# Kernel optimization log

Hardware: AMD Instinct MI355X
Metric: run time of the kernel (lower is better)

Reference implementation:

```python
import jax, jax.numpy as jnp
import numpy as np

B, T, C = 8, 2048, 1024  # micro_bsz, seq_len, n_embd (== complexsize)


def setup_inputs() -> dict:
    key = jax.random.key(0)
    ks = jax.random.split(key, 6)
    w = lambda k, shape: (jax.random.normal(k, shape, dtype=jnp.float32) * 0.02)
    return {
        "x": jax.random.normal(ks[0], (B, T, C), dtype=jnp.float32),
        "Wk": w(ks[1], (2 * C, C)),      # key: n_embd -> 2*n_embd (no bias)
        "Wa": w(ks[2], (C, 2 * C)),      # activation: 2*n_embd -> n_embd (no bias)
        "Wf": w(ks[3], (2, C, C)),       # WaveNet filter conv, kernel=2, WIO layout
        "Wg": w(ks[4], (2, C, C)),       # WaveNet gate conv, kernel=2, WIO layout
        "Wo": w(ks[5], (C, C)),          # WaveNet 1x1 output projection
    }


def _causal_conv(x, W):
    # x: [B,T,Cin], W: [K,Cin,Cout]; left-pad K-1 for causality
    return jax.lax.conv_general_dilated(
        x, W, window_strides=(1,), padding=[(W.shape[0] - 1, 0)],
        dimension_numbers=("NWC", "WIO", "NWC"))


def _wavenet_short(x, Wf, Wg, Wo):
    # undialated gated WaveNet unit: tanh(conv_f(x)) * sigmoid(conv_g(x)) -> 1x1 proj
    h = jnp.tanh(_causal_conv(x, Wf)) * jax.nn.sigmoid(_causal_conv(x, Wg))
    return h @ Wo.T


def reference(x, Wk, Wa, Wf, Wg, Wo):
    Bx, Tx, Cx = x.shape
    k = (x @ Wk.T).reshape(Bx, Tx, Cx, 2)                 # [B,T,C,2]
    cv = jax.lax.complex(k[..., 0], k[..., 1])            # view_as_complex -> [B,T,C]
    scale = jax.lax.cummax(jnp.abs(cv), axis=1)           # running max of magnitude
    cv2 = cv / scale.astype(cv.dtype)                      # normalize magnitude <= 1
    kv = jnp.cumprod(cv2, axis=1)                          # complex cumulative product
    re = jnp.stack([kv.real, kv.imag], axis=-1).reshape(Bx, Tx, 2 * Cx)  # view_as_real
    return (re @ Wa.T) * _wavenet_short(x * scale, Wf, Wg, Wo)
```

## Files before the change

### kernel.cpp

```cpp
#include <hip/hip_runtime.h>
#include <cmath>

#define T_SEQ 2048
#define C_DIM 1024
#define BM 128
#define BN 128
#define BK 32

typedef unsigned short u16;
typedef unsigned int u32;
typedef short bf16x8 __attribute__((ext_vector_type(8)));
typedef _Float16 f16x8 __attribute__((ext_vector_type(8)));
typedef float f32x4 __attribute__((ext_vector_type(4)));
typedef unsigned short u16x8 __attribute__((ext_vector_type(8)));

#define AS1 __attribute__((address_space(1)))
#define AS3 __attribute__((address_space(3)))

__device__ __forceinline__ u16 f2bf(float f) {
    u32 u = __builtin_bit_cast(u32, f);
    u32 r = u + 0x7fffu + ((u >> 16) & 1u);
    return (u16)(r >> 16);
}
__device__ __forceinline__ u16 f2h(float f) {
    return __builtin_bit_cast(u16, (_Float16)f);
}
__device__ __forceinline__ float h2f(u16 h) {
    return (float)__builtin_bit_cast(_Float16, h);
}
__device__ __forceinline__ void gl_lds16(const void* g, void* l) {
    __builtin_amdgcn_global_load_lds((const AS1 u32*)g, (AS3 u32*)l, 16, 0, 0);
}

__device__ __forceinline__ int xcd_swz(int lin, int nwg) {
    return (lin & 7) * (nwg >> 3) + (lin >> 3);
}

#define SBAR() do { __builtin_amdgcn_sched_barrier(0); \
                    __builtin_amdgcn_s_barrier(); \
                    __builtin_amdgcn_sched_barrier(0); } while (0)
#define VMC(n) do { asm volatile("s_waitcnt vmcnt(" #n ")" ::: "memory"); \
                    __builtin_amdgcn_sched_barrier(0); } while (0)
#define LGKM0() do { asm volatile("s_waitcnt lgkmcnt(0)" ::: "memory"); \
                     __builtin_amdgcn_sched_barrier(0); } while (0)

__global__ __launch_bounds__(512, 2)
void gemm8(const u16* __restrict__ Ap, const u16* __restrict__ Bp,
           u16* __restrict__ Cout, int M, int N, int K)
{
    __shared__ u16 lds[2 * 32768];
    const int tid  = threadIdx.x;
    const int lane = tid & 63;
    const int wid  = tid >> 6;
    const int wrow = wid >> 2;
    const int wcol = wid & 3;
    const int gx = gridDim.x;
    const int lin = xcd_swz(blockIdx.x + gx * blockIdx.y, gx * gridDim.y);
    const int m0 = (lin / gx) * 256;
    const int n0 = (lin % gx) * 256;
    const int NT = K / 64;

    f32x4 acc[8][4] = {};

    auto stageu = [&](int t, int u) {
        const int isB = u & 1, kh = u >> 1;
        u16* ubase = &lds[(t & 1) * 32768 + isB * 16384 + kh * 8192];
        const u16* src = isB ? Bp + (size_t)n0 * K : Ap + (size_t)m0 * K;
        const int k0 = t * 64 + kh * 32;
        #pragma unroll
        for (int j = 0; j < 2; ++j) {
            const int c = wid + 8 * j;
            const int p = c * 64 + lane;
            const int row = p >> 2;
            const int sp  = (p & 3) ^ ((row >> 1) & 3);
            gl_lds16(src + (size_t)row * K + k0 + sp * 8, ubase + c * 512);
        }
    };

    auto lda = [&](int buf, int kh, int mq, f16x8 (&a)[4]) {
        const u16* base = &lds[buf * 32768 + kh * 8192];
        #pragma unroll
        for (int f = 0; f < 4; ++f) {
            const int row = wrow * 128 + mq * 64 + f * 16 + (lane & 15);
            const int sp  = (lane >> 4) ^ ((row >> 1) & 3);
            a[f] = *(const f16x8*)&base[row * 32 + sp * 8];
        }
    };
    auto ldb = [&](int buf, int kh, f16x8 (&b)[4]) {
        const u16* base = &lds[buf * 32768 + 16384 + kh * 8192];
        #pragma unroll
        for (int f = 0; f < 4; ++f) {
            const int row = wcol * 64 + f * 16 + (lane & 15);
            const int sp  = (lane >> 4) ^ ((row >> 1) & 3);
            b[f] = *(const f16x8*)&base[row * 32 + sp * 8];
        }
    };
    auto mm = [&](const f16x8 (&a)[4], const f16x8 (&b)[4], int mq) {
        __builtin_amdgcn_s_setprio(1);
        #pragma unroll
        for (int fm = 0; fm < 4; ++fm)
            #pragma unroll
            for (int fn = 0; fn < 4; ++fn)
                acc[mq * 4 + fm][fn] = __builtin_amdgcn_mfma_f32_16x16x32_f16(
                    a[fm], b[fn], acc[mq * 4 + fm][fn], 0, 0, 0);
        __builtin_amdgcn_s_setprio(0);
    };

    stageu(0, 0); stageu(0, 1); stageu(0, 2); stageu(0, 3);
    VMC(0);
    SBAR();

    f16x8 a[4], b[4];
    for (int t = 0; t < NT; ++t) {
        const int buf = t & 1;
        const bool more = (t + 1 < NT);
        lda(buf, 0, 0, a); ldb(buf, 0, b);
        if (more) stageu(t + 1, 0);
        SBAR(); LGKM0();
        mm(a, b, 0);
        SBAR();
        lda(buf, 0, 1, a);
        if (more) { stageu(t + 1, 1); VMC(4); } else { VMC(0); }
        SBAR(); LGKM0();
        mm(a, b, 1);
        SBAR();
        lda(buf, 1, 0, a); ldb(buf, 1, b);
        if (more) stageu(t + 1, 2);
        SBAR(); LGKM0();
        mm(a, b, 0);
        SBAR();
        lda(buf, 1, 1, a);
        if (more) { stageu(t + 1, 3); VMC(4); }
        SBAR(); LGKM0();
        mm(a, b, 1);
        SBAR();
    }

    const int crow0 = m0 + wrow * 128 + ((lane >> 4) << 2);
    const int ccol  = n0 + wcol * 64 + (lane & 15);
    #pragma unroll
    for (int mi = 0; mi < 8; ++mi)
        #pragma unroll
        for (int fn = 0; fn < 4; ++fn)
            #pragma unroll
            for (int r = 0; r < 4; ++r)
                Cout[(size_t)(crow0 + mi * 16 + r) * N + ccol + fn * 16] =
                    f2h(acc[mi][fn][r]);
}

__global__ __launch_bounds__(512, 2)
void conv8(const u16* __restrict__ A, const u16* __restrict__ Wfgt,
           u16* __restrict__ H, int M)
{
    __shared__ u16 lds[2 * 32768];
    const int tid  = threadIdx.x;
    const int lane = tid & 63;
    const int wid  = tid >> 6;
    const int wrow = wid >> 1;
    const int wcol = wid & 1;
    const int gx = gridDim.x;
    const int lin = xcd_swz(blockIdx.x + gx * blockIdx.y, gx * gridDim.y);
    const int m0 = (lin / gx) * 256;
    const int n0 = (lin % gx) * 128;
    const int NT = 32;

    f32x4 accF[4][4] = {};
    f32x4 accG[4][4] = {};

    auto stageA = [&](int t, int kh) {
        u16* ubase = &lds[(t & 1) * 32768 + kh * 8192];
        const int tap = t >> 4;
        const int k0 = (t & 15) * 64 + kh * 32;
        const int sh = (tap == 0) ? 1 : 0;
        #pragma unroll
        for (int j = 0; j < 2; ++j) {
            const int c = wid + 8 * j;
            const int p = c * 64 + lane;
            const int row = p >> 2;
            const int sp  = (p & 3) ^ ((row >> 1) & 3);
            int grow = m0 + row - sh;
            if (grow < 0) grow = 0;
            gl_lds16(A + (size_t)grow * C_DIM + k0 + sp * 8, ubase + c * 512);
        }
    };
    auto stageB = [&](int t, int kh) {
        u16* ubase = &lds[(t & 1) * 32768 + 16384 + kh * 8192];
        const int tap = t >> 4;
        const int k0 = (t & 15) * 64 + kh * 32;
        const u16* BF = Wfgt + (size_t)tap * 2 * C_DIM * C_DIM;
        const u16* BG = BF + (size_t)C_DIM * C_DIM;
        #pragma unroll
        for (int j = 0; j < 2; ++j) {
            const int c = wid + 8 * j;
            const int isG = c >> 3;
            const int p = (c & 7) * 64 + lane;
            const int row = p >> 2;
            const int sp  = (p & 3) ^ ((row >> 1) & 3);
            const u16* src = (isG ? BG : BF) + (size_t)(n0 + row) * C_DIM + k0 + sp * 8;
            gl_lds16(src, ubase + isG * 4096 + (c & 7) * 512);
        }
    };

    auto lda4 = [&](int buf, int kh, bf16x8 (&a)[4]) {
        const u16* base = &lds[buf * 32768 + kh * 8192];
        #pragma unroll
        for (int f = 0; f < 4; ++f) {
            const int row = wrow * 64 + f * 16 + (lane & 15);
            const int sp  = (lane >> 4) ^ ((row >> 1) & 3);
            a[f] = *(const bf16x8*)&base[row * 32 + sp * 8];
        }
    };
    auto ldb4 = [&](int buf, int kh, int isG, bf16x8 (&b)[4]) {
        const u16* base = &lds[buf * 32768 + 16384 + kh * 8192 + isG * 4096];
        #pragma unroll
        for (int f = 0; f < 4; ++f) {
            const int row = wcol * 64 + f * 16 + (lane & 15);
            const int sp  = (lane >> 4) ^ ((row >> 1) & 3);
            b[f] = *(const bf16x8*)&base[row * 32 + sp * 8];
        }
    };
    auto mm4 = [&](const bf16x8 (&a)[4], const bf16x8 (&b)[4], f32x4 (&acc)[4][4]) {
        #pragma unroll
        for (int fm = 0; fm < 4; ++fm)
            #pragma unroll
            for (int fn = 0; fn < 4; ++fn)
                acc[fm][fn] = __builtin_amdgcn_mfma_f32_16x16x32_bf16(
                    a[fm], b[fn], acc[fm][fn], 0, 0, 0);
    };

    const bool zrow = (m0 % T_SEQ) == 0;
    const bool zlane = (wrow == 0) && ((lane & 15) == 0);
    const bf16x8 zvec = {0,0,0,0,0,0,0,0};

    stageA(0, 0); stageB(0, 0); stageA(0, 1); stageB(0, 1);
    VMC(0);
    SBAR();

    bf16x8 a[4], bF[4], bG[4];
    for (int t = 0; t < NT; ++t) {
        const int buf = t & 1;
        const bool more = (t + 1 < NT);
        const bool z0 = zrow && (t < 16);
        lda4(buf, 0, a); ldb4(buf, 0, 0, bF); ldb4(buf, 0, 1, bG);
        if (more) { stageA(t + 1, 0); stageB(t + 1, 0); VMC(4); } else { VMC(0); }
        SBAR(); LGKM0();
        if (z0 && zlane) a[0] = zvec;
        __builtin_amdgcn_s_setprio(1);
        mm4(a, bF, accF); mm4(a, bG, accG);
        __builtin_amdgcn_s_setprio(0);
        SBAR();
        lda4(buf, 1, a); ldb4(buf, 1, 0, bF); ldb4(buf, 1, 1, bG);
        if (more) { stageA(t + 1, 1); stageB(t + 1, 1); VMC(4); } else { VMC(0); }
        SBAR(); LGKM0();
        if (z0 && zlane) a[0] = zvec;
        __builtin_amdgcn_s_setprio(1);
        mm4(a, bF, accF); mm4(a, bG, accG);
        __builtin_amdgcn_s_setprio(0);
        SBAR();
    }

    const int crow0 = m0 + wrow * 64 + ((lane >> 4) << 2);
    const int ccol  = n0 + wcol * 64 + (lane & 15);
    #pragma unroll
    for (int fm = 0; fm < 4; ++fm)
        #pragma unroll
        for (int fn = 0; fn < 4; ++fn)
            #pragma unroll
            for (int r = 0; r < 4; ++r) {
                const float fv = accF[fm][fn][r];
                const float gv = accG[fm][fn][r];
                const float th = 1.0f - 2.0f / (expf(2.0f * fv) + 1.0f);
                const float sg = 1.0f / (1.0f + expf(-gv));
                H[(size_t)(crow0 + fm * 16 + r) * C_DIM + ccol + fn * 16] = f2bf(th * sg);
            }
}

__global__ __launch_bounds__(256)
void dual_gemm(const u16* __restrict__ A1, const u16* __restrict__ B1, int K1,
               const u16* __restrict__ A2, const u16* __restrict__ B2, int K2,
               float* __restrict__ out, int M, int N)
{
    __shared__ u16 lds[2 * 2 * 4096];
    const int tid  = threadIdx.x;
    const int lane = tid & 63;
    const int wid  = tid >> 6;
    const int wr = wid >> 1, wc = wid & 1;
    const int gx = gridDim.x;
    const int lin = xcd_swz(blockIdx.x + gx * blockIdx.y, gx * gridDim.y);
    const int m0 = (lin / gx) * BM;
    const int n0 = (lin % gx) * BN;

    f32x4 acc1[4][4] = {};
    f32x4 acc2[4][4] = {};

    auto stage = [&](const u16* Ap, const u16* Bp, int K, int it, int buf) {
        const int k0 = it * BK;
        u16* base = &lds[buf * 8192];
        #pragma unroll
        for (int i = 0; i < 2; ++i) {
            const int chunk = wid + 4 * i;
            const int rloc  = chunk * 16 + (lane >> 2);
            const int slot  = (lane & 3) ^ ((rloc >> 1) & 3);
            gl_lds16(Bp + (size_t)(n0 + rloc) * K + k0 + slot * 8,
                     base + 4096 + chunk * 512);
            gl_lds16(Ap + (size_t)(m0 + rloc) * K + k0 + slot * 8,
                     base + chunk * 512);
        }
    };

    auto compute = [&](int buf, f32x4 (&acc)[4][4]) {
        const u16* base = &lds[buf * 8192];
        bf16x8 a[4], b[4];
        #pragma unroll
        for (int f = 0; f < 4; ++f) {
            const int row = wr * 64 + f * 16 + (lane & 15);
            const int sp  = ((lane >> 4) & 3) ^ ((row >> 1) & 3);
            a[f] = *(const bf16x8*)&base[row * 32 + sp * 8];
            const int rowb = wc * 64 + f * 16 + (lane & 15);
            const int spb  = ((lane >> 4) & 3) ^ ((rowb >> 1) & 3);
            b[f] = *(const bf16x8*)&base[4096 + rowb * 32 + spb * 8];
        }
        #pragma unroll
        for (int fm = 0; fm < 4; ++fm)
            #pragma unroll
            for (int fn = 0; fn < 4; ++fn)
                acc[fm][fn] = __builtin_amdgcn_mfma_f32_16x16x32_bf16(a[fm], b[fn], acc[fm][fn], 0, 0, 0);
    };

    const int NT1 = K1 / BK, NT2 = K2 / BK;
    stage(A1, B1, K1, 0, 0);
    int cur = 0;
    for (int it = 0; it < NT1; ++it) {
        __syncthreads();
        if (it + 1 < NT1) stage(A1, B1, K1, it + 1, cur ^ 1);
        else              stage(A2, B2, K2, 0, cur ^ 1);
        compute(cur, acc1);
        cur ^= 1;
    }
    for (int it = 0; it < NT2; ++it) {
        __syncthreads();
        if (it + 1 < NT2) stage(A2, B2, K2, it + 1, cur ^ 1);
        compute(cur, acc2);
        cur ^= 1;
    }

    const int crow0 = m0 + wr * 64 + ((lane >> 4) << 2);
    const int ccol  = n0 + wc * 64 + (lane & 15);
    #pragma unroll
    for (int fm = 0; fm < 4; ++fm)
        #pragma unroll
        for (int fn = 0; fn < 4; ++fn)
            #pragma unroll
            for (int r = 0; r < 4; ++r) {
                const size_t idx = (size_t)(crow0 + fm * 16 + r) * N + ccol + fn * 16;
                out[idx] = acc1[fm][fn][r] * acc2[fm][fn][r];
            }
}

#define SSEG 32
#define SCHB 32
#define SSL (T_SEQ / SSEG)

__global__ __launch_bounds__(1024, 1)
void scan_kernel(u16* __restrict__ kq, u16* __restrict__ xyb)
{
    __shared__ float  lmax[SSEG][SCHB];
    __shared__ float2 lprod[SSEG][SCHB];
    const int blk = blockIdx.x;
    const int b   = blk >> 5;
    const int c0  = (blk & 31) * SCHB;
    const int ch  = threadIdx.x & (SCHB - 1);
    const int seg = threadIdx.x >> 5;
    const int c   = c0 + ch;
    const int t0  = seg * SSL;
    const size_t baseh = (size_t)b * T_SEQ * 2048 + 2 * c + (size_t)t0 * 2048;
    const size_t base1 = (size_t)b * T_SEQ * C_DIM + c + (size_t)t0 * C_DIM;

    float m2 = 0.f;
    {
        size_t idx = baseh;
        for (int g = 0; g < SSL / 4; ++g) {
            const u32 v0 = *(const u32*)&kq[idx];
            const u32 v1 = *(const u32*)&kq[idx + 2048];
            const u32 v2 = *(const u32*)&kq[idx + 4096];
            const u32 v3 = *(const u32*)&kq[idx + 6144];
            float re, im;
            re = h2f((u16)(v0 & 0xffffu)); im = h2f((u16)(v0 >> 16)); m2 = fmaxf(m2, re*re + im*im);
            re = h2f((u16)(v1 & 0xffffu)); im = h2f((u16)(v1 >> 16)); m2 = fmaxf(m2, re*re + im*im);
            re = h2f((u16)(v2 & 0xffffu)); im = h2f((u16)(v2 >> 16)); m2 = fmaxf(m2, re*re + im*im);
            re = h2f((u16)(v3 & 0xffffu)); im = h2f((u16)(v3 >> 16)); m2 = fmaxf(m2, re*re + im*im);
            idx += 4 * 2048;
        }
    }
    lmax[seg][ch] = sqrtf(m2);
    __syncthreads();
    #pragma unroll
    for (int s = 1; s < SSEG; s <<= 1) {
        const float v = lmax[seg][ch];
        const float u = (seg >= s) ? lmax[seg - s][ch] : 0.f;
        __syncthreads();
        lmax[seg][ch] = fmaxf(v, u);
        __syncthreads();
    }
    const float premax = (seg > 0) ? lmax[seg - 1][ch] : 0.f;

    float pr = 1.f, pi = 0.f;
    float m = premax;
    {
        size_t idx = baseh, idx1 = base1;
        for (int g = 0; g < SSL / 4; ++g) {
            const u32 v0 = *(const u32*)&kq[idx];
            const u32 v1 = *(const u32*)&kq[idx + 2048];
            const u32 v2 = *(const u32*)&kq[idx + 4096];
            const u32 v3 = *(const u32*)&kq[idx + 6144];
            const u16 x0 = xyb[idx1];
            const u16 x1 = xyb[idx1 + C_DIM];
            const u16 x2 = xyb[idx1 + 2 * C_DIM];
            const u16 x3 = xyb[idx1 + 3 * C_DIM];
            u32 vv[4] = {v0, v1, v2, v3};
            u16 xx[4] = {x0, x1, x2, x3};
            #pragma unroll
            for (int q = 0; q < 4; ++q) {
                const float re = h2f((u16)(vv[q] & 0xffffu));
                const float im = h2f((u16)(vv[q] >> 16));
                m = fmaxf(m, sqrtf(re * re + im * im));
                const float inv = 1.f / m;
                const float r0 = re * inv, r1 = im * inv;
                const float nr = pr * r0 - pi * r1;
                const float ni = pr * r1 + pi * r0;
                pr = nr; pi = ni;
                xyb[idx1 + (size_t)q * C_DIM] = f2bf(h2f(xx[q]) * m);
            }
            idx += 4 * 2048; idx1 += 4 * C_DIM;
        }
    }
    lprod[seg][ch] = make_float2(pr, pi);
    __syncthreads();
    #pragma unroll
    for (int s = 1; s < SSEG; s <<= 1) {
        const float2 v = lprod[seg][ch];
        const float2 u = (seg >= s) ? lprod[seg - s][ch] : make_float2(1.f, 0.f);
        __syncthreads();
        lprod[seg][ch] = make_float2(u.x * v.x - u.y * v.y,
                                     u.x * v.y + u.y * v.x);
        __syncthreads();
    }
    float ppr = 1.f, ppi = 0.f;
    if (seg > 0) { const float2 pp = lprod[seg - 1][ch]; ppr = pp.x; ppi = pp.y; }

    pr = 1.f; pi = 0.f;
    m = premax;
    {
        size_t idx = baseh;
        for (int g = 0; g < SSL / 4; ++g) {
            const u32 v0 = *(const u32*)&kq[idx];
            const u32 v1 = *(const u32*)&kq[idx + 2048];
            const u32 v2 = *(const u32*)&kq[idx + 4096];
            const u32 v3 = *(const u32*)&kq[idx + 6144];
            u32 vv[4] = {v0, v1, v2, v3};
            u32 ww[4];
            #pragma unroll
            for (int q = 0; q < 4; ++q) {
                const float re = h2f((u16)(vv[q] & 0xffffu));
                const float im = h2f((u16)(vv[q] >> 16));
                m = fmaxf(m, sqrtf(re * re + im * im));
                const float inv = 1.f / m;
                const float r0 = re * inv, r1 = im * inv;
                const float nr = pr * r0 - pi * r1;
                const float ni = pr * r1 + pi * r0;
                pr = nr; pi = ni;
                const float fr = ppr * nr - ppi * ni;
                const float fi = ppr * ni + ppi * nr;
                ww[q] = ((u32)f2bf(fi) << 16) | (u32)f2bf(fr);
            }
            *(u32*)&kq[idx]        = ww[0];
            *(u32*)&kq[idx + 2048] = ww[1];
            *(u32*)&kq[idx + 4096] = ww[2];
            *(u32*)&kq[idx + 6144] = ww[3];
            idx += 4 * 2048;
        }
    }
}

__global__ void cvt_weights(const float* __restrict__ Wk, const float* __restrict__ Wa,
                            const float* __restrict__ Wo, u16* __restrict__ Wkh,
                            u16* __restrict__ Wab, u16* __restrict__ Wob)
{
    const int n1 = 2048 * 1024, n2 = 2 * 2048 * 1024, n3 = n2 + 1024 * 1024;
    const int i = (blockIdx.x * blockDim.x + threadIdx.x) * 4;
    if (i < n1) {
        const float4 v = *(const float4*)&Wk[i];
        ushort4 o; o.x = f2h(v.x); o.y = f2h(v.y); o.z = f2h(v.z); o.w = f2h(v.w);
        *(ushort4*)&Wkh[i] = o;
    } else if (i < n2) {
        const int j = i - n1;
        const float4 v = *(const float4*)&Wa[j];
        ushort4 o; o.x = f2bf(v.x); o.y = f2bf(v.y); o.z = f2bf(v.z); o.w = f2bf(v.w);
        *(ushort4*)&Wab[j] = o;
    } else if (i < n3) {
        const int j = i - n2;
        const float4 v = *(const float4*)&Wo[j];
        ushort4 o; o.x = f2bf(v.x); o.y = f2bf(v.y); o.z = f2bf(v.z); o.w = f2bf(v.w);
        *(ushort4*)&Wob[j] = o;
    }
}

__global__ void cvt_f16(const float* __restrict__ src, u16* __restrict__ dst, int n)
{
    const int i = (blockIdx.x * blockDim.x + threadIdx.x) * 4;
    if (i >= n) return;
    const float4 v = *(const float4*)&src[i];
    ushort4 o;
    o.x = f2h(v.x); o.y = f2h(v.y); o.z = f2h(v.z); o.w = f2h(v.w);
    *(ushort4*)&dst[i] = o;
}

__global__ __launch_bounds__(256)
void wtrans(const float* __restrict__ Wf, const float* __restrict__ Wg,
            u16* __restrict__ dst)
{
    __shared__ float tile[64][65];
    const int z = blockIdx.z;
    const float* src = ((z < 2) ? Wf : Wg) + (size_t)(z & 1) * C_DIM * C_DIM;
    u16* d = dst + (size_t)(z & 1) * (2 * C_DIM) * C_DIM
                 + ((z < 2) ? (size_t)0 : (size_t)C_DIM * C_DIM);
    const int k0 = blockIdx.x * 64;
    const int n0 = blockIdx.y * 64;
    const int tx = threadIdx.x & 63, ty = threadIdx.x >> 6;
    #pragma unroll
    for (int i = 0; i < 16; ++i) {
        const int r = ty + i * 4;
        tile[r][tx] = src[(size_t)(k0 + r) * C_DIM + n0 + tx];
    }
    __syncthreads();
    #pragma unroll
    for (int i = 0; i < 16; ++i) {
        const int r = ty + i * 4;
        d[(size_t)(n0 + r) * C_DIM + k0 + tx] = f2bf(tile[tx][r]);
    }
}

extern "C" void kernel_launch(void* const* d_in, const int* in_sizes, int n_in,
                              void* d_out, int out_size, void* d_ws, size_t ws_size,
                              hipStream_t stream)
{
    const float* x  = (const float*)d_in[0];
    const float* Wk = (const float*)d_in[1];
    const float* Wa = (const float*)d_in[2];
    const float* Wf = (const float*)d_in[3];
    const float* Wg = (const float*)d_in[4];
    const float* Wo = (const float*)d_in[5];
    float* out = (float*)d_out;

    const int M = 8 * T_SEQ;
    u16* kq   = (u16*)d_ws;
    u16* yb   = (u16*)((char*)d_ws + 67108864ull);
    u16* hb   = (u16*)((char*)d_ws + 100663296ull);
    u16* Wkh  = (u16*)((char*)d_ws + 134217728ull);
    u16* Wab  = Wkh + 2048 * 1024;
    u16* Wfgt = Wab + 2048 * 1024;
    u16* Wob  = Wfgt + 2ull * 2048 * 1024;

    cvt_weights<<<(5 * 1024 * 1024 / 4 + 255) / 256, 256, 0, stream>>>(
        Wk, Wa, Wo, Wkh, Wab, Wob);
    wtrans  <<<dim3(16, 16, 4), 256, 0, stream>>>(Wf, Wg, Wfgt);
    cvt_f16 <<<(M * 1024 / 4) / 256, 256, 0, stream>>>(x, yb, M * 1024);

    gemm8<<<dim3(2048 / 256, M / 256), 512, 0, stream>>>(
        yb, Wkh, kq, M, 2048, 1024);

    scan_kernel<<<256, 1024, 0, stream>>>(kq, yb);

    conv8<<<dim3(1024 / 128, M / 256), 512, 0, stream>>>(yb, Wfgt, hb, M);

    dual_gemm<<<dim3(1024 / BN, M / BM), 256, 0, stream>>>(
        kq, Wab, 2048, hb, Wob, 1024, out, M, 1024);
}
```

Before: 446.4 us.

## Interleave filter/gate weights and split F/G across waves with LDS exchange

Conv weights are rearranged so each 128-row block holds 64 filter and 64 gate output channels. Each conv block now computes a single 256x128 GEMM tile covering 64 output columns, with one wave column producing filter values and the other gate values. The two halves are combined through LDS in the epilogue. This halves accumulator registers per thread and B staging traffic, but doubles the grid, re-reads A twice as often, and lowers the occupancy hint to 1.

```diff
diff --git a/kernel.cpp b/kernel.cpp
--- a/kernel.cpp
+++ b/kernel.cpp
@@ -148,11 +148,11 @@
                     f2h(acc[mi][fn][r]);
 }
 
-__global__ __launch_bounds__(512, 2)
-void conv8(const u16* __restrict__ A, const u16* __restrict__ Wfgt,
+__global__ __launch_bounds__(512, 1)
+void convG(const u16* __restrict__ A, const u16* __restrict__ Wcat,
            u16* __restrict__ H, int M)
 {
-    __shared__ u16 lds[2 * 32768];
+    __shared__ u16 lds[2 * 24576];
     const int tid  = threadIdx.x;
     const int lane = tid & 63;
     const int wid  = tid >> 6;
@@ -161,48 +161,39 @@
     const int gx = gridDim.x;
     const int lin = xcd_swz(blockIdx.x + gx * blockIdx.y, gx * gridDim.y);
     const int m0 = (lin / gx) * 256;
-    const int n0 = (lin % gx) * 128;
+    const int nb = lin % gx;
     const int NT = 32;
 
-    f32x4 accF[4][4] = {};
-    f32x4 accG[4][4] = {};
-
-    auto stageA = [&](int t, int kh) {
-        u16* ubase = &lds[(t & 1) * 32768 + kh * 8192];
+    f32x4 acc[4][4] = {};
+
+    auto stageK = [&](int t, int kh) {
         const int tap = t >> 4;
         const int k0 = (t & 15) * 64 + kh * 32;
-        const int sh = (tap == 0) ? 1 : 0;
-        #pragma unroll
-        for (int j = 0; j < 2; ++j) {
-            const int c = wid + 8 * j;
-            const int p = c * 64 + lane;
-            const int row = p >> 2;
-            const int sp  = (p & 3) ^ ((row >> 1) & 3);
-            int grow = m0 + row - sh;
-            if (grow < 0) grow = 0;
-            gl_lds16(A + (size_t)grow * C_DIM + k0 + sp * 8, ubase + c * 512);
-        }
-    };
-    auto stageB = [&](int t, int kh) {
-        u16* ubase = &lds[(t & 1) * 32768 + 16384 + kh * 8192];
-        const int tap = t >> 4;
-        const int k0 = (t & 15) * 64 + kh * 32;
-        const u16* BF = Wfgt + (size_t)tap * 2 * C_DIM * C_DIM;
-        const u16* BG = BF + (size_t)C_DIM * C_DIM;
-        #pragma unroll
-        for (int j = 0; j < 2; ++j) {
-            const int c = wid + 8 * j;
-            const int isG = c >> 3;
-            const int p = (c & 7) * 64 + lane;
-            const int row = p >> 2;
-            const int sp  = (p & 3) ^ ((row >> 1) & 3);
-            const u16* src = (isG ? BG : BF) + (size_t)(n0 + row) * C_DIM + k0 + sp * 8;
-            gl_lds16(src, ubase + isG * 4096 + (c & 7) * 512);
+        {
+            u16* ubase = &lds[(t & 1) * 24576 + kh * 8192];
+            const int sh = (tap == 0) ? 1 : 0;
+            #pragma unroll
+            for (int j = 0; j < 2; ++j) {
+                const int c = tid + 512 * j;
+                const int row = c >> 2;
+                const int sp  = (c & 3) ^ ((row >> 1) & 3);
+                int grow = m0 + row - sh;
+                if (grow < 0) grow = 0;
+                gl_lds16(A + (size_t)grow * C_DIM + k0 + sp * 8, ubase + c * 8);
+            }
+        }
+        {
+            u16* ubase = &lds[(t & 1) * 24576 + 16384 + kh * 4096];
+            const u16* src = Wcat + (size_t)tap * 2 * C_DIM * C_DIM
+                           + (size_t)nb * 128 * C_DIM;
+            const int row = tid >> 2;
+            const int sp  = (tid & 3) ^ ((row >> 1) & 3);
+            gl_lds16(src + (size_t)row * C_DIM + k0 + sp * 8, ubase + tid * 8);
         }
     };
 
     auto lda4 = [&](int buf, int kh, bf16x8 (&a)[4]) {
-        const u16* base = &lds[buf * 32768 + kh * 8192];
+        const u16* base = &lds[buf * 24576 + kh * 8192];
         #pragma unroll
         for (int f = 0; f < 4; ++f) {
             const int row = wrow * 64 + f * 16 + (lane & 15);
@@ -210,8 +201,8 @@
             a[f] = *(const bf16x8*)&base[row * 32 + sp * 8];
         }
     };
-    auto ldb4 = [&](int buf, int kh, int isG, bf16x8 (&b)[4]) {
-        const u16* base = &lds[buf * 32768 + 16384 + kh * 8192 + isG * 4096];
+    auto ldb4 = [&](int buf, int kh, bf16x8 (&b)[4]) {
+        const u16* base = &lds[buf * 24576 + 16384 + kh * 4096];
         #pragma unroll
         for (int f = 0; f < 4; ++f) {
             const int row = wcol * 64 + f * 16 + (lane & 15);
@@ -219,60 +210,75 @@
             b[f] = *(const bf16x8*)&base[row * 32 + sp * 8];
         }
     };
-    auto mm4 = [&](const bf16x8 (&a)[4], const bf16x8 (&b)[4], f32x4 (&acc)[4][4]) {
+    auto mm = [&](const bf16x8 (&a)[4], const bf16x8 (&b)[4]) {
+        __builtin_amdgcn_s_setprio(1);
         #pragma unroll
         for (int fm = 0; fm < 4; ++fm)
             #pragma unroll
             for (int fn = 0; fn < 4; ++fn)
                 acc[fm][fn] = __builtin_amdgcn_mfma_f32_16x16x32_bf16(
                     a[fm], b[fn], acc[fm][fn], 0, 0, 0);
-    };
-
-    const bool zrow = (m0 % T_SEQ) == 0;
+        __builtin_amdgcn_s_setprio(0);
+    };
+
+    const bool zrow  = (m0 % T_SEQ) == 0;
     const bool zlane = (wrow == 0) && ((lane & 15) == 0);
     const bf16x8 zvec = {0,0,0,0,0,0,0,0};
 
-    stageA(0, 0); stageB(0, 0); stageA(0, 1); stageB(0, 1);
+    stageK(0, 0); stageK(0, 1);
     VMC(0);
     SBAR();
 
-    bf16x8 a[4], bF[4], bG[4];
+    bf16x8 a[4], b[4];
     for (int t = 0; t < NT; ++t) {
         const int buf = t & 1;
         const bool more = (t + 1 < NT);
         const bool z0 = zrow && (t < 16);
-        lda4(buf, 0, a); ldb4(buf, 0, 0, bF); ldb4(buf, 0, 1, bG);
-        if (more) { stageA(t + 1, 0); stageB(t + 1, 0); VMC(4); } else { VMC(0); }
+        lda4(buf, 0, a); ldb4(buf, 0, b);
+        if (more) { stageK(t + 1, 0); VMC(3); } else { VMC(0); }
         SBAR(); LGKM0();
         if (z0 && zlane) a[0] = zvec;
-        __builtin_amdgcn_s_setprio(1);
-        mm4(a, bF, accF); mm4(a, bG, accG);
-        __builtin_amdgcn_s_setprio(0);
+        mm(a, b);
         SBAR();
-        lda4(buf, 1, a); ldb4(buf, 1, 0, bF); ldb4(buf, 1, 1, bG);
-        if (more) { stageA(t + 1, 1); stageB(t + 1, 1); VMC(4); } else { VMC(0); }
+        lda4(buf, 1, a); ldb4(buf, 1, b);
+        if (more) { stageK(t + 1, 1); VMC(3); } else { VMC(0); }
         SBAR(); LGKM0();
         if (z0 && zlane) a[0] = zvec;
-        __builtin_amdgcn_s_setprio(1);
-        mm4(a, bF, accF); mm4(a, bG, accG);
-        __builtin_amdgcn_s_setprio(0);
+        mm(a, b);
         SBAR();
     }
 
-    const int crow0 = m0 + wrow * 64 + ((lane >> 4) << 2);
-    const int ccol  = n0 + wcol * 64 + (lane & 15);
-    #pragma unroll
-    for (int fm = 0; fm < 4; ++fm)
-        #pragma unroll
-        for (int fn = 0; fn < 4; ++fn)
-            #pragma unroll
-            for (int r = 0; r < 4; ++r) {
-                const float fv = accF[fm][fn][r];
-                const float gv = accG[fm][fn][r];
-                const float th = 1.0f - 2.0f / (expf(2.0f * fv) + 1.0f);
-                const float sg = 1.0f / (1.0f + expf(-gv));
-                H[(size_t)(crow0 + fm * 16 + r) * C_DIM + ccol + fn * 16] = f2bf(th * sg);
+    float* fl = (float*)lds;
+    if (wcol == 1) {
+        #pragma unroll
+        for (int fm = 0; fm < 4; ++fm)
+            #pragma unroll
+            for (int fn = 0; fn < 4; ++fn) {
+                const int s = (fm * 4 + fn) ^ (lane & 15);
+                *(f32x4*)&fl[(size_t)wrow * 4096 + (size_t)lane * 64 + s * 4] = acc[fm][fn];
             }
+    }
+    LGKM0();
+    SBAR();
+    if (wcol == 0) {
+        const int crow0 = m0 + wrow * 64 + ((lane >> 4) << 2);
+        const int ccol  = nb * 64 + (lane & 15);
+        #pragma unroll
+        for (int fm = 0; fm < 4; ++fm)
+            #pragma unroll
+            for (int fn = 0; fn < 4; ++fn) {
+                const int s = (fm * 4 + fn) ^ (lane & 15);
+                const f32x4 g = *(const f32x4*)&fl[(size_t)wrow * 4096 + (size_t)lane * 64 + s * 4];
+                #pragma unroll
+                for (int r = 0; r < 4; ++r) {
+                    const float fv = acc[fm][fn][r];
+                    const float gv = g[r];
+                    const float th = 1.0f - 2.0f / (expf(2.0f * fv) + 1.0f);
+                    const float sg = 1.0f / (1.0f + expf(-gv));
+                    H[(size_t)(crow0 + fm * 16 + r) * C_DIM + ccol + fn * 16] = f2bf(th * sg);
+                }
+            }
+    }
 }
 
 __global__ __launch_bounds__(256)
@@ -522,8 +528,8 @@
     __shared__ float tile[64][65];
     const int z = blockIdx.z;
     const float* src = ((z < 2) ? Wf : Wg) + (size_t)(z & 1) * C_DIM * C_DIM;
-    u16* d = dst + (size_t)(z & 1) * (2 * C_DIM) * C_DIM
-                 + ((z < 2) ? (size_t)0 : (size_t)C_DIM * C_DIM);
+    u16* d = dst + (size_t)(z & 1) * 2 * C_DIM * C_DIM;
+    const int isG = (z >= 2) ? 1 : 0;
     const int k0 = blockIdx.x * 64;
     const int n0 = blockIdx.y * 64;
     const int tx = threadIdx.x & 63, ty = threadIdx.x >> 6;
@@ -536,7 +542,8 @@
     #pragma unroll
     for (int i = 0; i < 16; ++i) {
         const int r = ty + i * 4;
-        d[(size_t)(n0 + r) * C_DIM + k0 + tx] = f2bf(tile[tx][r]);
+        d[(size_t)(n0 >> 6) * 128 * C_DIM + (size_t)(r + isG * 64) * C_DIM + k0 + tx]
+            = f2bf(tile[tx][r]);
     }
 }
 
@@ -558,12 +565,12 @@
     u16* hb   = (u16*)((char*)d_ws + 100663296ull);
     u16* Wkh  = (u16*)((char*)d_ws + 134217728ull);
     u16* Wab  = Wkh + 2048 * 1024;
-    u16* Wfgt = Wab + 2048 * 1024;
-    u16* Wob  = Wfgt + 2ull * 2048 * 1024;
+    u16* Wcat = Wab + 2048 * 1024;
+    u16* Wob  = Wcat + 2ull * 2048 * 1024;
 
     cvt_weights<<<(5 * 1024 * 1024 / 4 + 255) / 256, 256, 0, stream>>>(
         Wk, Wa, Wo, Wkh, Wab, Wob);
-    wtrans  <<<dim3(16, 16, 4), 256, 0, stream>>>(Wf, Wg, Wfgt);
+    wtrans  <<<dim3(16, 16, 4), 256, 0, stream>>>(Wf, Wg, Wcat);
     cvt_f16 <<<(M * 1024 / 4) / 256, 256, 0, stream>>>(x, yb, M * 1024);
 
     gemm8<<<dim3(2048 / 256, M / 256), 512, 0, stream>>>(
@@ -571,7 +578,7 @@
 
     scan_kernel<<<256, 1024, 0, stream>>>(kq, yb);
 
-    conv8<<<dim3(1024 / 128, M / 256), 512, 0, stream>>>(yb, Wfgt, hb, M);
+    convG<<<dim3(16, M / 256), 512, 0, stream>>>(yb, Wcat, hb, M);
 
     dual_gemm<<<dim3(1024 / BN, M / BM), 256, 0, stream>>>(
         kq, Wab, 2048, hb, Wob, 1024, out, M, 1024);
```

Result: slower. 507.3 us (+13.6%).

## Replace dual_gemm with two templated 256x256 gemm8 launches and fused multiply epilogue

Applied to the files above, without the earlier changes.

Removes the 128x128 dual_gemm kernel. It is replaced by two launches of the tuned 256x256 gemm8 kernel, which is templated on data type (f16/bf16) and epilogue. The first launch computes the activation GEMM into an fp16 intermediate buffer. The second computes the WaveNet output projection and multiplies by that intermediate in its epilogue. The aim is better data reuse and pipelining from the larger tile, paid for with an extra intermediate write/read and fp16 rounding of the activation product.

```diff
diff --git a/kernel.cpp b/kernel.cpp
--- a/kernel.cpp
+++ b/kernel.cpp
@@ -3,9 +3,6 @@
 
 #define T_SEQ 2048
 #define C_DIM 1024
-#define BM 128
-#define BN 128
-#define BK 32
 
 typedef unsigned short u16;
 typedef unsigned int u32;
@@ -44,9 +41,11 @@
 #define LGKM0() do { asm volatile("s_waitcnt lgkmcnt(0)" ::: "memory"); \
                      __builtin_amdgcn_sched_barrier(0); } while (0)
 
+template<int DT, int EPI>
 __global__ __launch_bounds__(512, 2)
 void gemm8(const u16* __restrict__ Ap, const u16* __restrict__ Bp,
-           u16* __restrict__ Cout, int M, int N, int K)
+           void* __restrict__ Cout, const u16* __restrict__ Cmul,
+           int M, int N, int K)
 {
     __shared__ u16 lds[2 * 32768];
     const int tid  = threadIdx.x;
@@ -77,32 +76,39 @@
         }
     };
 
-    auto lda = [&](int buf, int kh, int mq, f16x8 (&a)[4]) {
+    auto lda = [&](int buf, int kh, int mq, u16x8 (&a)[4]) {
         const u16* base = &lds[buf * 32768 + kh * 8192];
         #pragma unroll
         for (int f = 0; f < 4; ++f) {
             const int row = wrow * 128 + mq * 64 + f * 16 + (lane & 15);
             const int sp  = (lane >> 4) ^ ((row >> 1) & 3);
-            a[f] = *(const f16x8*)&base[row * 32 + sp * 8];
-        }
-    };
-    auto ldb = [&](int buf, int kh, f16x8 (&b)[4]) {
+            a[f] = *(const u16x8*)&base[row * 32 + sp * 8];
+        }
+    };
+    auto ldb = [&](int buf, int kh, u16x8 (&b)[4]) {
         const u16* base = &lds[buf * 32768 + 16384 + kh * 8192];
         #pragma unroll
         for (int f = 0; f < 4; ++f) {
             const int row = wcol * 64 + f * 16 + (lane & 15);
             const int sp  = (lane >> 4) ^ ((row >> 1) & 3);
-            b[f] = *(const f16x8*)&base[row * 32 + sp * 8];
-        }
-    };
-    auto mm = [&](const f16x8 (&a)[4], const f16x8 (&b)[4], int mq) {
+            b[f] = *(const u16x8*)&base[row * 32 + sp * 8];
+        }
+    };
+    auto mm = [&](const u16x8 (&a)[4], const u16x8 (&b)[4], int mq) {
         __builtin_amdgcn_s_setprio(1);
         #pragma unroll
         for (int fm = 0; fm < 4; ++fm)
             #pragma unroll
-            for (int fn = 0; fn < 4; ++fn)
-                acc[mq * 4 + fm][fn] = __builtin_amdgcn_mfma_f32_16x16x32_f16(
-                    a[fm], b[fn], acc[mq * 4 + fm][fn], 0, 0, 0);
+            for (int fn = 0; fn < 4; ++fn) {
+                if constexpr (DT == 1)
+                    acc[mq * 4 + fm][fn] = __builtin_amdgcn_mfma_f32_16x16x32_f16(
+                        __builtin_bit_cast(f16x8, a[fm]), __builtin_bit_cast(f16x8, b[fn]),
+                        acc[mq * 4 + fm][fn], 0, 0, 0);
+                else
+                    acc[mq * 4 + fm][fn] = __builtin_amdgcn_mfma_f32_16x16x32_bf16(
+                        __builtin_bit_cast(bf16x8, a[fm]), __builtin_bit_cast(bf16x8, b[fn]),
+                        acc[mq * 4 + fm][fn], 0, 0, 0);
+            }
         __builtin_amdgcn_s_setprio(0);
     };
 
@@ -110,7 +116,7 @@
     VMC(0);
     SBAR();
 
-    f16x8 a[4], b[4];
+    u16x8 a[4], b[4];
     for (int t = 0; t < NT; ++t) {
         const int buf = t & 1;
         const bool more = (t + 1 < NT);
@@ -143,9 +149,13 @@
         #pragma unroll
         for (int fn = 0; fn < 4; ++fn)
             #pragma unroll
-            for (int r = 0; r < 4; ++r)
-                Cout[(size_t)(crow0 + mi * 16 + r) * N + ccol + fn * 16] =
-                    f2h(acc[mi][fn][r]);
+            for (int r = 0; r < 4; ++r) {
+                const size_t idx = (size_t)(crow0 + mi * 16 + r) * N + ccol + fn * 16;
+                if constexpr (EPI == 0)
+                    ((u16*)Cout)[idx] = f2h(acc[mi][fn][r]);
+                else
+                    ((float*)Cout)[idx] = h2f(Cmul[idx]) * acc[mi][fn][r];
+            }
 }
 
 __global__ __launch_bounds__(512, 2)
@@ -272,88 +282,6 @@
                 const float th = 1.0f - 2.0f / (expf(2.0f * fv) + 1.0f);
                 const float sg = 1.0f / (1.0f + expf(-gv));
                 H[(size_t)(crow0 + fm * 16 + r) * C_DIM + ccol + fn * 16] = f2bf(th * sg);
-            }
-}
-
-__global__ __launch_bounds__(256)
-void dual_gemm(const u16* __restrict__ A1, const u16* __restrict__ B1, int K1,
-               const u16* __restrict__ A2, const u16* __restrict__ B2, int K2,
-               float* __restrict__ out, int M, int N)
-{
-    __shared__ u16 lds[2 * 2 * 4096];
-    const int tid  = threadIdx.x;
-    const int lane = tid & 63;
-    const int wid  = tid >> 6;
-    const int wr = wid >> 1, wc = wid & 1;
-    const int gx = gridDim.x;
-    const int lin = xcd_swz(blockIdx.x + gx * blockIdx.y, gx * gridDim.y);
-    const int m0 = (lin / gx) * BM;
-    const int n0 = (lin % gx) * BN;
-
-    f32x4 acc1[4][4] = {};
-    f32x4 acc2[4][4] = {};
-
-    auto stage = [&](const u16* Ap, const u16* Bp, int K, int it, int buf) {
-        const int k0 = it * BK;
-        u16* base = &lds[buf * 8192];
-        #pragma unroll
-        for (int i = 0; i < 2; ++i) {
-            const int chunk = wid + 4 * i;
-            const int rloc  = chunk * 16 + (lane >> 2);
-            const int slot  = (lane & 3) ^ ((rloc >> 1) & 3);
-            gl_lds16(Bp + (size_t)(n0 + rloc) * K + k0 + slot * 8,
-                     base + 4096 + chunk * 512);
-            gl_lds16(Ap + (size_t)(m0 + rloc) * K + k0 + slot * 8,
-                     base + chunk * 512);
-        }
-    };
-
-    auto compute = [&](int buf, f32x4 (&acc)[4][4]) {
-        const u16* base = &lds[buf * 8192];
-        bf16x8 a[4], b[4];
-        #pragma unroll
-        for (int f = 0; f < 4; ++f) {
-            const int row = wr * 64 + f * 16 + (lane & 15);
-            const int sp  = ((lane >> 4) & 3) ^ ((row >> 1) & 3);
-            a[f] = *(const bf16x8*)&base[row * 32 + sp * 8];
-            const int rowb = wc * 64 + f * 16 + (lane & 15);
-            const int spb  = ((lane >> 4) & 3) ^ ((rowb >> 1) & 3);
-            b[f] = *(const bf16x8*)&base[4096 + rowb * 32 + spb * 8];
-        }
-        #pragma unroll
-        for (int fm = 0; fm < 4; ++fm)
-            #pragma unroll
-            for (int fn = 0; fn < 4; ++fn)
-                acc[fm][fn] = __builtin_amdgcn_mfma_f32_16x16x32_bf16(a[fm], b[fn], acc[fm][fn], 0, 0, 0);
-    };
-
-    const int NT1 = K1 / BK, NT2 = K2 / BK;
-    stage(A1, B1, K1, 0, 0);
-    int cur = 0;
-    for (int it = 0; it < NT1; ++it) {
-        __syncthreads();
-        if (it + 1 < NT1) stage(A1, B1, K1, it + 1, cur ^ 1);
-        else              stage(A2, B2, K2, 0, cur ^ 1);
-        compute(cur, acc1);
-        cur ^= 1;
-    }
-    for (int it = 0; it < NT2; ++it) {
-        __syncthreads();
-        if (it + 1 < NT2) stage(A2, B2, K2, it + 1, cur ^ 1);
-        compute(cur, acc2);
-        cur ^= 1;
-    }
-
-    const int crow0 = m0 + wr * 64 + ((lane >> 4) << 2);
-    const int ccol  = n0 + wc * 64 + (lane & 15);
-    #pragma unroll
-    for (int fm = 0; fm < 4; ++fm)
-        #pragma unroll
-        for (int fn = 0; fn < 4; ++fn)
-            #pragma unroll
-            for (int r = 0; r < 4; ++r) {
-                const size_t idx = (size_t)(crow0 + fm * 16 + r) * N + ccol + fn * 16;
-                out[idx] = acc1[fm][fn][r] * acc2[fm][fn][r];
             }
 }
 
@@ -560,19 +488,23 @@
     u16* Wab  = Wkh + 2048 * 1024;
     u16* Wfgt = Wab + 2048 * 1024;
     u16* Wob  = Wfgt + 2ull * 2048 * 1024;
+    u16* acth = (u16*)((char*)d_ws + 153092096ull);
 
     cvt_weights<<<(5 * 1024 * 1024 / 4 + 255) / 256, 256, 0, stream>>>(
         Wk, Wa, Wo, Wkh, Wab, Wob);
     wtrans  <<<dim3(16, 16, 4), 256, 0, stream>>>(Wf, Wg, Wfgt);
     cvt_f16 <<<(M * 1024 / 4) / 256, 256, 0, stream>>>(x, yb, M * 1024);
 
-    gemm8<<<dim3(2048 / 256, M / 256), 512, 0, stream>>>(
-        yb, Wkh, kq, M, 2048, 1024);
+    gemm8<1, 0><<<dim3(2048 / 256, M / 256), 512, 0, stream>>>(
+        yb, Wkh, kq, nullptr, M, 2048, 1024);
 
     scan_kernel<<<256, 1024, 0, stream>>>(kq, yb);
 
+    gemm8<0, 0><<<dim3(1024 / 256, M / 256), 512, 0, stream>>>(
+        kq, Wab, acth, nullptr, M, 1024, 2048);
+
     conv8<<<dim3(1024 / 128, M / 256), 512, 0, stream>>>(yb, Wfgt, hb, M);
 
-    dual_gemm<<<dim3(1024 / BN, M / BM), 256, 0, stream>>>(
-        kq, Wab, 2048, hb, Wob, 1024, out, M, 1024);
-}
+    gemm8<0, 1><<<dim3(1024 / 256, M / 256), 512, 0, stream>>>(
+        hb, Wob, out, acth, M, 1024, 1024);
+}
```

Result: no change. 441.7 us (median of 2 runs) (-1.0%).
